# Performance work log

Hardware: AMD Instinct MI355X
Metric: run time of the kernel (lower is better)

The kernel has to match this reference:

```python
import jax, jax.numpy as jnp
import numpy as np

B, T, N, C, H, S = 8, 24, 2048, 64, 8, 4
HD = C // H
EPS_NORM = 1e-12   # torch F.normalize eps
EPS_DEN = 1e-5     # clamp_min in fast_attention
LN_EPS = 1e-5
SCALE1 = 0.01      # self.scale[1]


def _ln(x, g, b):
    m = x.mean(-1, keepdims=True)
    v = ((x - m) ** 2).mean(-1, keepdims=True)
    return (x - m) * jax.lax.rsqrt(v + LN_EPS) * g + b


def _fast_attn(q, k, v):
    # q,k,v: [b, l, h, m] ; performer-style linear attention with L2-normalized feature maps
    q = q / jnp.maximum(jnp.linalg.norm(q, axis=-1, keepdims=True), EPS_NORM)
    k = k / jnp.maximum(jnp.linalg.norm(k, axis=-1, keepdims=True), EPS_NORM)
    L = q.shape[1]
    kvs = jnp.einsum('blhm,blhd->bhmd', k, v)
    num = jnp.einsum('bnhm,bhmd->bnhd', q, kvs) + L * v
    den = jnp.einsum('bnhm,bhm->bnh', q, k.sum(axis=1))[..., None] + L
    return num / jnp.maximum(den, EPS_DEN)  # [b, l, h, d]


def _attn_layer(x, qkv_w, out_w, out_b):
    # x: [B, T, N, C]; spatial (over N) + temporal (over T) linear attention, concat, project
    b, t, n, c = x.shape
    qkv = x @ qkv_w.T                      # [b,t,n,3c], no bias (qkv_bias=False)
    q, k, v = jnp.split(qkv, 3, axis=-1)
    sh = lambda a: a.reshape(b * t, n, H, HD)                    # flatten (B,T) -> attend over nodes
    th = lambda a: a.swapaxes(1, 2).reshape(b * n, t, H, HD)     # flatten (B,N) -> attend over time
    out_s = _fast_attn(sh(q), sh(k), sh(v)).reshape(b, t, n, c)
    out_t = _fast_attn(th(q), th(k), th(v)).reshape(b, n, t, c).swapaxes(1, 2)
    return jnp.concatenate([out_s, out_t], axis=-1) @ out_w.T + out_b


def setup_inputs() -> dict:
    key = jax.random.key(0)
    ks = jax.random.split(key, 20)
    stdv = 1.0 / np.sqrt(N)
    w = 0.02
    inp = {
        'x': jax.random.normal(ks[0], (B, T, N, C), jnp.float32),
        'phi': jax.random.normal(ks[1], (S, N, N), jnp.float32) * (N ** -0.5),
        'phi_inv': jax.random.normal(ks[2], (S, N, N), jnp.float32) * (N ** -0.5),
        'diag_w': jax.random.uniform(ks[3], (S, N), jnp.float32, -stdv, stdv),
        'qkv0_w': jax.random.normal(ks[4], (3 * C, C), jnp.float32) * w,
        'out0_w': jax.random.normal(ks[5], (C, 2 * C), jnp.float32) * w,
        'out0_b': jnp.zeros((C,), jnp.float32),
        'qkv1_w': jax.random.normal(ks[6], (3 * C, C), jnp.float32) * w,
        'out1_w': jax.random.normal(ks[7], (C, 2 * C), jnp.float32) * w,
        'out1_b': jnp.zeros((C,), jnp.float32),
        'pw0_w': jax.random.normal(ks[8], (C, C), jnp.float32) * w,
        'pw0_b': jax.random.normal(ks[9], (C,), jnp.float32) * w,
        'pw1_w': jax.random.normal(ks[10], (C, C), jnp.float32) * w,
        'pw1_b': jax.random.normal(ks[11], (C,), jnp.float32) * w,
        'fc1_w': jax.random.normal(ks[12], (2 * C, C), jnp.float32) * w,
        'fc1_b': jnp.zeros((2 * C,), jnp.float32),
        'fc2_w': jax.random.normal(ks[13], (C, 2 * C), jnp.float32) * w,
        'fc2_b': jnp.zeros((C,), jnp.float32),
        'ln1_g': jnp.ones((C,), jnp.float32),
        'ln1_b': jnp.zeros((C,), jnp.float32),
        'ln2_g': jnp.ones((C,), jnp.float32),
        'ln2_b': jnp.zeros((C,), jnp.float32),
    }
    return inp


def reference(x, phi, phi_inv, diag_w, qkv0_w, out0_w, out0_b, qkv1_w, out1_w, out1_b,
              pw0_w, pw0_b, pw1_w, pw1_b, fc1_w, fc1_b, fc2_w, fc2_b,
              ln1_g, ln1_b, ln2_g, ln2_b):
    # Graph wavelet propagate (order=2): x_list = [x, W(x)] with
    # W(x)[b,t,n,c] = sum_j (sum_s phi_s diag(diag_w_s) phi_inv_s)[n,j] x[b,t,j,c]
    Msum = jnp.einsum('sij,sj,sjk->ik', phi, diag_w, phi_inv)   # [N,N]
    x_k = jnp.einsum('nj,btjc->btnc', Msum, x)
    att0 = _attn_layer(x, qkv0_w, out0_w, out0_b)
    att1 = _attn_layer(x_k, qkv1_w, out1_w, out1_b)
    # scale = [1, 0.01]; c starts as x, then becomes att0
    x_glo = x + att0 * (x @ pw0_w.T + pw0_b) + att1 * (att0 @ pw1_w.T + pw1_b) * SCALE1
    # In torch, x_glo aliases x (in-place +=), so ln1(x + x_glo) == ln1(2 * x_glo)
    y = _ln(2.0 * x_glo, ln1_g, ln1_b)
    h = jax.nn.relu(y @ fc1_w.T + fc1_b) @ fc2_w.T + fc2_b
    return _ln(y + h, ln2_g, ln2_b)
```

## Files before the change

kernel.cpp:

```cpp
#include <hip/hip_runtime.h>

typedef unsigned short u16;
typedef unsigned int u32;
typedef __attribute__((ext_vector_type(8))) __bf16 bf16x8;
typedef __attribute__((ext_vector_type(4))) float floatx4;

#define TB 24
#define NN 2048
#define QC 192

__device__ __forceinline__ float b2f(u16 v) { return __uint_as_float(((u32)v) << 16); }
__device__ __forceinline__ u16 f2bu(float f) {
  u32 u = __float_as_uint(f);
  u32 r = (u + 0x7fffu + ((u >> 16) & 1u)) >> 16;
  return (u16)r;
}
__device__ __forceinline__ u32 packpair(float a, float b) {
  return (u32)f2bu(a) | ((u32)f2bu(b) << 16);
}
__device__ __forceinline__ void unpack8(uint4 v, float* f) {
  f[0] = __uint_as_float(v.x << 16); f[1] = __uint_as_float(v.x & 0xffff0000u);
  f[2] = __uint_as_float(v.y << 16); f[3] = __uint_as_float(v.y & 0xffff0000u);
  f[4] = __uint_as_float(v.z << 16); f[5] = __uint_as_float(v.z & 0xffff0000u);
  f[6] = __uint_as_float(v.w << 16); f[7] = __uint_as_float(v.w & 0xffff0000u);
}
__device__ __forceinline__ float wredsum(float v) {
#pragma unroll
  for (int m = 32; m > 0; m >>= 1) v += __shfl_xor(v, m, 64);
  return v;
}

__global__ __launch_bounds__(256) void cast_weights(
    const float* __restrict__ q0, const float* __restrict__ q1,
    const float* __restrict__ o0, const float* __restrict__ o1,
    const float* __restrict__ p0, const float* __restrict__ p1,
    const float* __restrict__ f1, const float* __restrict__ f2,
    u16* __restrict__ dst) {
  int i = blockIdx.x * 256 + threadIdx.x;
  float v;
  if (i < 12288) v = q0[i];
  else if (i < 24576) v = q1[i - 12288];
  else if (i < 32768) v = o0[i - 24576];
  else if (i < 40960) v = o1[i - 32768];
  else if (i < 45056) v = p0[i - 40960];
  else if (i < 49152) v = p1[i - 45056];
  else if (i < 57344) v = f1[i - 49152];
  else v = f2[i - 57344];
  dst[i] = f2bu(v);
}

__global__ __launch_bounds__(256) void cast_bulk(const float* __restrict__ src,
                                                 u16* __restrict__ dst) {
  long i = ((long)blockIdx.x * 256 + threadIdx.x) * 8;
  float4 a = *(const float4*)(src + i);
  float4 b = *(const float4*)(src + i + 4);
  uint4 o = uint4{packpair(a.x, a.y), packpair(a.z, a.w),
                  packpair(b.x, b.y), packpair(b.z, b.w)};
  *(uint4*)(dst + i) = o;
}

__global__ __launch_bounds__(256) void prep_pt(const float* __restrict__ phi_inv,
                                               const float* __restrict__ diag,
                                               u16* __restrict__ PT) {
  const int s = blockIdx.z;
  const float* phi_inv_s = phi_inv + (long)s * 4194304;
  const float* diag_s = diag + (long)s * 2048;
  u16* PTs = PT + (long)s * 4194304;
  const long i0 = (long)blockIdx.x * 64, j0 = (long)blockIdx.y * 64;
  __shared__ float tile[64][65];
  for (int t = threadIdx.x; t < 512; t += 256) {
    int r = t >> 3, c8 = (t & 7) << 3;
    float dv = diag_s[j0 + r];
    const float* sp = phi_inv_s + (j0 + r) * 2048 + i0 + c8;
    float4 p = *(const float4*)sp;
    float4 q = *(const float4*)(sp + 4);
    tile[r][c8 + 0] = p.x * dv; tile[r][c8 + 1] = p.y * dv;
    tile[r][c8 + 2] = p.z * dv; tile[r][c8 + 3] = p.w * dv;
    tile[r][c8 + 4] = q.x * dv; tile[r][c8 + 5] = q.y * dv;
    tile[r][c8 + 6] = q.z * dv; tile[r][c8 + 7] = q.w * dv;
  }
  __syncthreads();
  for (int t = threadIdx.x; t < 512; t += 256) {
    int r = t >> 3, c8 = (t & 7) << 3;
    uint4 o;
    o.x = packpair(tile[c8 + 0][r], tile[c8 + 1][r]);
    o.y = packpair(tile[c8 + 2][r], tile[c8 + 3][r]);
    o.z = packpair(tile[c8 + 4][r], tile[c8 + 5][r]);
    o.w = packpair(tile[c8 + 6][r], tile[c8 + 7][r]);
    *(uint4*)(PTs + (i0 + r) * 2048 + j0 + c8) = o;
  }
}

__global__ __launch_bounds__(256) void prep_xt(const float* __restrict__ x,
                                               u16* __restrict__ XT) {
  const int bt = blockIdx.y;
  const long j0 = (long)blockIdx.x * 64;
  __shared__ float tile[64][65];
  const float* src = x + (long)bt * NN * 64;
  for (int t = threadIdx.x; t < 512; t += 256) {
    int r = t >> 3, c8 = (t & 7) << 3;
    const float* sp = src + (j0 + r) * 64 + c8;
    float4 p = *(const float4*)sp;
    float4 q = *(const float4*)(sp + 4);
    tile[r][c8 + 0] = p.x; tile[r][c8 + 1] = p.y;
    tile[r][c8 + 2] = p.z; tile[r][c8 + 3] = p.w;
    tile[r][c8 + 4] = q.x; tile[r][c8 + 5] = q.y;
    tile[r][c8 + 6] = q.z; tile[r][c8 + 7] = q.w;
  }
  __syncthreads();
  u16* dst = XT + (long)bt * 64 * NN;
  for (int t = threadIdx.x; t < 512; t += 256) {
    int r = t >> 3, c8 = (t & 7) << 3;
    uint4 o;
    o.x = packpair(tile[c8 + 0][r], tile[c8 + 1][r]);
    o.y = packpair(tile[c8 + 2][r], tile[c8 + 3][r]);
    o.z = packpair(tile[c8 + 4][r], tile[c8 + 5][r]);
    o.w = packpair(tile[c8 + 6][r], tile[c8 + 7][r]);
    *(uint4*)(dst + (long)r * 2048 + j0 + c8) = o;
  }
}

template <int MODE>
__global__ __launch_bounds__(256) void gemm128(
    const u16* __restrict__ A, const u16* __restrict__ Bt, void* __restrict__ C,
    int K, int lda, int ldb, int ldc, int nseg, long aseg, long bseg) {
  __shared__ __align__(16) u16 As[128 * 64];
  __shared__ __align__(16) u16 Bs[128 * 64];
  const int tid = threadIdx.x;
  const int wave = tid >> 6, lane = tid & 63;
  const int l15 = lane & 15, lq = lane >> 4;
  const int wr = wave >> 1, wc = wave & 1;
  const long m0 = (long)blockIdx.x * 128;
  const long n0 = (long)blockIdx.y * 128;
  const int rl = lane >> 3;
  const int csw = (lane & 7) ^ rl;
  floatx4 acc[4][4];
#pragma unroll
  for (int a = 0; a < 4; a++)
#pragma unroll
    for (int b = 0; b < 4; b++) acc[a][b] = floatx4{0.f, 0.f, 0.f, 0.f};
  for (int s = 0; s < nseg; s++) {
    const u16* Ab = A + s * aseg;
    const u16* Bb = Bt + s * bseg;
    for (int k0 = 0; k0 < K; k0 += 64) {
      __syncthreads();
#pragma unroll
      for (int la = 0; la < 4; la++) {
        const int ldx = wave * 4 + la;
        const int rowt = ldx * 8 + rl;
        const u16* ga = Ab + (m0 + rowt) * (long)lda + k0 + csw * 8;
        const u16* gb = Bb + (n0 + rowt) * (long)ldb + k0 + csw * 8;
        __builtin_amdgcn_global_load_lds(
            (const __attribute__((address_space(1))) void*)ga,
            (__attribute__((address_space(3))) void*)(As + ldx * 512), 16, 0, 0);
        __builtin_amdgcn_global_load_lds(
            (const __attribute__((address_space(1))) void*)gb,
            (__attribute__((address_space(3))) void*)(Bs + ldx * 512), 16, 0, 0);
      }
      __syncthreads();
#pragma unroll
      for (int ks = 0; ks < 2; ks++) {
        bf16x8 af[4], bf[4];
        const int cp = ((ks * 4 + lq) ^ (l15 & 7)) * 8;
#pragma unroll
        for (int t = 0; t < 4; t++) {
          af[t] = *(const bf16x8*)(As + (wr * 64 + t * 16 + l15) * 64 + cp);
          bf[t] = *(const bf16x8*)(Bs + (wc * 64 + t * 16 + l15) * 64 + cp);
        }
#pragma unroll
        for (int ti = 0; ti < 4; ti++)
#pragma unroll
          for (int tj = 0; tj < 4; tj++)
            acc[ti][tj] = __builtin_amdgcn_mfma_f32_16x16x32_bf16(
                af[ti], bf[tj], acc[ti][tj], 0, 0, 0);
      }
    }
  }
#pragma unroll
  for (int ti = 0; ti < 4; ti++) {
#pragma unroll
    for (int tj = 0; tj < 4; tj++) {
#pragma unroll
      for (int i = 0; i < 4; i++) {
        const long row = m0 + wr * 64 + ti * 16 + lq * 4 + i;
        const long col = n0 + wc * 64 + tj * 16 + l15;
        if (MODE == 0) {
          ((u16*)C)[row * ldc + col] = f2bu(acc[ti][tj][i]);
        } else {
          ((float*)C)[(col >> 6) * 131072L + row * 64 + (col & 63)] = acc[ti][tj][i];
        }
      }
    }
  }
}

template <bool AF32, bool CF32>
__global__ __launch_bounds__(256) void gemm_bt(
    const void* __restrict__ A, const u16* __restrict__ Bt, void* __restrict__ C,
    int K, int lda, int ldb, int ldc, int nseg, long aseg, long bseg,
    long bbstride, long cbstride, int accum) {
  __shared__ __align__(16) u16 Asm[64][72];
  __shared__ __align__(16) u16 Bsm[64][72];
  const int tid = threadIdx.x;
  const int wave = tid >> 6, lane = tid & 63;
  const int l15 = lane & 15, lq = lane >> 4;
  const long m0 = (long)blockIdx.x * 64;
  const long n0 = (long)blockIdx.y * 64;
  const long bz = blockIdx.z;
  const int srow = tid >> 3;
  const int scol = (tid & 7) << 3;
  floatx4 acc[4];
#pragma unroll
  for (int t = 0; t < 4; t++) acc[t] = floatx4{0.f, 0.f, 0.f, 0.f};
  for (int s = 0; s < nseg; s++) {
    const u16* Bb = Bt + s * bseg + bz * bbstride;
    for (int k0 = 0; k0 < K; k0 += 64) {
      __syncthreads();
      uint4 a0, a1;
      if (AF32) {
        const float* Af = (const float*)A + s * aseg;
        const float* p0 = Af + (m0 + srow) * lda + k0 + scol;
        const float* p1 = Af + (m0 + srow + 32) * lda + k0 + scol;
        float4 x0 = *(const float4*)p0, x1 = *(const float4*)(p0 + 4);
        float4 y0 = *(const float4*)p1, y1 = *(const float4*)(p1 + 4);
        a0 = uint4{packpair(x0.x, x0.y), packpair(x0.z, x0.w),
                   packpair(x1.x, x1.y), packpair(x1.z, x1.w)};
        a1 = uint4{packpair(y0.x, y0.y), packpair(y0.z, y0.w),
                   packpair(y1.x, y1.y), packpair(y1.z, y1.w)};
      } else {
        const u16* Ab = (const u16*)A + s * aseg;
        a0 = *(const uint4*)(Ab + (m0 + srow) * lda + k0 + scol);
        a1 = *(const uint4*)(Ab + (m0 + srow + 32) * lda + k0 + scol);
      }
      uint4 b0 = *(const uint4*)(Bb + (n0 + srow) * ldb + k0 + scol);
      uint4 b1 = *(const uint4*)(Bb + (n0 + srow + 32) * ldb + k0 + scol);
      *(uint4*)(&Asm[srow][scol]) = a0;
      *(uint4*)(&Asm[srow + 32][scol]) = a1;
      *(uint4*)(&Bsm[srow][scol]) = b0;
      *(uint4*)(&Bsm[srow + 32][scol]) = b1;
      __syncthreads();
#pragma unroll
      for (int ks = 0; ks < 2; ks++) {
        bf16x8 af = *(const bf16x8*)(&Asm[wave * 16 + l15][ks * 32 + lq * 8]);
#pragma unroll
        for (int t = 0; t < 4; t++) {
          bf16x8 bfr = *(const bf16x8*)(&Bsm[t * 16 + l15][ks * 32 + lq * 8]);
          acc[t] = __builtin_amdgcn_mfma_f32_16x16x32_bf16(af, bfr, acc[t], 0, 0, 0);
        }
      }
    }
  }
#pragma unroll
  for (int t = 0; t < 4; t++) {
#pragma unroll
    for (int i = 0; i < 4; i++) {
      long off = (m0 + wave * 16 + lq * 4 + i) * ldc + n0 + t * 16 + l15;
      float v = acc[t][i];
      if (CF32) {
        float* Cb = (float*)C + bz * cbstride;
        if (accum) v += Cb[off];
        Cb[off] = v;
      } else {
        u16* Cb = (u16*)C + bz * cbstride;
        if (accum) v += b2f(Cb[off]);
        Cb[off] = f2bu(v);
      }
    }
  }
}

template <int K, int LDA, int NOUT, int LDO, bool BIAS, bool RELU, bool AF32, bool OF32>
__global__ __launch_bounds__(256) void skinny_gemm(const void* __restrict__ In,
                                                   const u16* __restrict__ W,
                                                   const float* __restrict__ Bv,
                                                   void* __restrict__ Out) {
  constexpr int NT = NOUT / 16;
  const int lane = threadIdx.x & 63;
  const int wave = threadIdx.x >> 6;
  const int l15 = lane & 15, lq = lane >> 4;
  const long m0 = ((long)blockIdx.x * 4 + wave) * 16;
  floatx4 acc[NT];
#pragma unroll
  for (int t = 0; t < NT; t++) acc[t] = floatx4{0.f, 0.f, 0.f, 0.f};
#pragma unroll
  for (int k0 = 0; k0 < K; k0 += 32) {
    bf16x8 af;
    if (AF32) {
      const float* arow = (const float*)In + (m0 + l15) * (long)LDA + lq * 8;
      float4 p = *(const float4*)(arow + k0);
      float4 q = *(const float4*)(arow + k0 + 4);
      uint4 pk = uint4{packpair(p.x, p.y), packpair(p.z, p.w),
                       packpair(q.x, q.y), packpair(q.z, q.w)};
      af = __builtin_bit_cast(bf16x8, pk);
    } else {
      const u16* arow = (const u16*)In + (m0 + l15) * (long)LDA + lq * 8;
      af = *(const bf16x8*)(arow + k0);
    }
#pragma unroll
    for (int t = 0; t < NT; t++) {
      bf16x8 bfr = *(const bf16x8*)(W + (t * 16 + l15) * K + k0 + lq * 8);
      acc[t] = __builtin_amdgcn_mfma_f32_16x16x32_bf16(af, bfr, acc[t], 0, 0, 0);
    }
  }
#pragma unroll
  for (int t = 0; t < NT; t++) {
    float bv = BIAS ? Bv[t * 16 + l15] : 0.f;
#pragma unroll
    for (int i = 0; i < 4; i++) {
      float v = acc[t][i] + bv;
      if (RELU) v = fmaxf(v, 0.f);
      long off = (m0 + lq * 4 + i) * (long)LDO + t * 16 + l15;
      if (OF32) ((float*)Out)[off] = v;
      else ((u16*)Out)[off] = f2bu(v);
    }
  }
}

__global__ __launch_bounds__(256) void spat_stats(const u16* __restrict__ Q,
                                                  float* __restrict__ stats) {
  const int bh = blockIdx.x;
  const int bt = bh >> 3, h = bh & 7;
  const int tid = threadIdx.x, lane = tid & 63, wave = tid >> 6;
  float kvs[8][8], ksm[8];
#pragma unroll
  for (int m = 0; m < 8; m++) {
    ksm[m] = 0.f;
#pragma unroll
    for (int d = 0; d < 8; d++) kvs[m][d] = 0.f;
  }
  const u16* base = Q + (long)bt * NN * QC + 64 + h * 8;
  for (int l = tid; l < NN; l += 256) {
    const u16* p = base + (long)l * QC;
    float kv[8], vv[8];
    unpack8(*(const uint4*)p, kv);
    unpack8(*(const uint4*)(p + 64), vv);
    float nr = 0.f;
#pragma unroll
    for (int m = 0; m < 8; m++) nr += kv[m] * kv[m];
    float inv = 1.f / fmaxf(sqrtf(nr), 1e-12f);
#pragma unroll
    for (int m = 0; m < 8; m++) {
      float km = kv[m] * inv;
      ksm[m] += km;
#pragma unroll
      for (int d = 0; d < 8; d++) kvs[m][d] += km * vv[d];
    }
  }
  __shared__ float red[4][72];
#pragma unroll
  for (int m = 0; m < 8; m++) {
    ksm[m] = wredsum(ksm[m]);
#pragma unroll
    for (int d = 0; d < 8; d++) kvs[m][d] = wredsum(kvs[m][d]);
  }
  if (lane == 0) {
#pragma unroll
    for (int m = 0; m < 8; m++) {
      red[wave][64 + m] = ksm[m];
#pragma unroll
      for (int d = 0; d < 8; d++) red[wave][m * 8 + d] = kvs[m][d];
    }
  }
  __syncthreads();
  if (tid < 72) {
    stats[(long)bh * 72 + tid] = red[0][tid] + red[1][tid] + red[2][tid] + red[3][tid];
  }
}

__global__ __launch_bounds__(256) void temp_attn(u16* __restrict__ Q) {
  const long g = (long)blockIdx.x * 256 + threadIdx.x;
  const int h = (int)(g & 7);
  const long bn = g >> 3;
  const int n = (int)(bn & 2047);
  const int b = (int)(bn >> 11);
  u16* qb = Q + ((long)b * TB * NN + n) * QC + h * 8;
  const long ts = (long)NN * QC;
  float kvs[8][8], ksm[8];
#pragma unroll
  for (int m = 0; m < 8; m++) {
    ksm[m] = 0.f;
#pragma unroll
    for (int d = 0; d < 8; d++) kvs[m][d] = 0.f;
  }
  for (int t = 0; t < TB; t++) {
    const u16* p = qb + t * ts;
    float kv[8], vv[8];
    unpack8(*(const uint4*)(p + 64), kv);
    unpack8(*(const uint4*)(p + 128), vv);
    float nr = 0.f;
#pragma unroll
    for (int m = 0; m < 8; m++) nr += kv[m] * kv[m];
    float inv = 1.f / fmaxf(sqrtf(nr), 1e-12f);
#pragma unroll
    for (int m = 0; m < 8; m++) {
      float km = kv[m] * inv;
      ksm[m] += km;
#pragma unroll
      for (int d = 0; d < 8; d++) kvs[m][d] += km * vv[d];
    }
  }
  for (int t = 0; t < TB; t++) {
    u16* p = qb + t * ts;
    float qv[8], vv[8];
    unpack8(*(const uint4*)p, qv);
    unpack8(*(const uint4*)(p + 128), vv);
    float nr = 0.f;
#pragma unroll
    for (int m = 0; m < 8; m++) nr += qv[m] * qv[m];
    float inv = 1.f / fmaxf(sqrtf(nr), 1e-12f);
    float num[8];
    float den = 24.f;
#pragma unroll
    for (int d = 0; d < 8; d++) num[d] = 24.f * vv[d];
#pragma unroll
    for (int m = 0; m < 8; m++) {
      float qm = qv[m] * inv;
      den += qm * ksm[m];
#pragma unroll
      for (int d = 0; d < 8; d++) num[d] += qm * kvs[m][d];
    }
    den = fmaxf(den, 1e-5f);
    float id = 1.f / den;
    uint4 o;
    o.x = packpair(num[0] * id, num[1] * id);
    o.y = packpair(num[2] * id, num[3] * id);
    o.z = packpair(num[4] * id, num[5] * id);
    o.w = packpair(num[6] * id, num[7] * id);
    *(uint4*)(p + 64) = o;
  }
}

__global__ __launch_bounds__(256) void spat_out(u16* __restrict__ Q,
                                                const float* __restrict__ stats) {
  const long g = (long)blockIdx.x * 256 + threadIdx.x;
  const int h = (int)(g & 7);
  const long r = g >> 3;
  const int bt = (int)(r >> 11);
  u16* p = Q + r * QC + h * 8;
  float qv[8], vv[8];
  unpack8(*(const uint4*)p, qv);
  unpack8(*(const uint4*)(p + 128), vv);
  const float* st = stats + ((long)bt * 8 + h) * 72;
  float nr = 0.f;
#pragma unroll
  for (int m = 0; m < 8; m++) nr += qv[m] * qv[m];
  float inv = 1.f / fmaxf(sqrtf(nr), 1e-12f);
  const float L = 2048.f;
  float num[8];
#pragma unroll
  for (int d = 0; d < 8; d++) num[d] = L * vv[d];
  float den = L;
#pragma unroll
  for (int m = 0; m < 8; m++) {
    float qm = qv[m] * inv;
    den += qm * st[64 + m];
#pragma unroll
    for (int d = 0; d < 8; d++) num[d] += qm * st[m * 8 + d];
  }
  den = fmaxf(den, 1e-5f);
  float id = 1.f / den;
  uint4 o;
  o.x = packpair(num[0] * id, num[1] * id);
  o.y = packpair(num[2] * id, num[3] * id);
  o.z = packpair(num[4] * id, num[5] * id);
  o.w = packpair(num[6] * id, num[7] * id);
  *(uint4*)p = o;
}

__global__ __launch_bounds__(256) void combine_ln(
    const float* __restrict__ x, const u16* __restrict__ a0p, int sa0,
    const float* __restrict__ a1p, const u16* __restrict__ P0, int sp0,
    const u16* __restrict__ P1, int sp1, const float* __restrict__ g1,
    const float* __restrict__ b1, u16* __restrict__ Y) {
  const long r = (long)blockIdx.x * 4 + (threadIdx.x >> 6);
  const int d = threadIdx.x & 63;
  float xv = x[r * 64 + d];
  float a0 = b2f(a0p[r * sa0 + d]);
  float a1 = a1p[r * 64 + d];
  float p0 = b2f(P0[r * sp0 + d]);
  float p1 = b2f(P1[r * sp1 + d]);
  float t = 2.f * (xv + a0 * p0 + a1 * p1 * 0.01f);
  float mu = wredsum(t) * 0.015625f;
  float dv = t - mu;
  float var = wredsum(dv * dv) * 0.015625f;
  float y = dv * rsqrtf(var + 1e-5f) * g1[d] + b1[d];
  Y[r * 64 + d] = f2bu(y);
}

__global__ __launch_bounds__(256) void final_ln(const u16* __restrict__ Yp,
                                                const u16* __restrict__ Op,
                                                const float* __restrict__ g2,
                                                const float* __restrict__ b2p,
                                                float* __restrict__ out) {
  const long r = (long)blockIdx.x * 4 + (threadIdx.x >> 6);
  const int d = threadIdx.x & 63;
  const long o = r * 64 + d;
  float t = b2f(Yp[o]) + b2f(Op[o]);
  float mu = wredsum(t) * 0.015625f;
  float dv = t - mu;
  float var = wredsum(dv * dv) * 0.015625f;
  out[o] = dv * rsqrtf(var + 1e-5f) * g2[d] + b2p[d];
}

extern "C" void kernel_launch(void* const* d_in, const int* in_sizes, int n_in,
                              void* d_out, int out_size, void* d_ws, size_t ws_size,
                              hipStream_t stream) {
  const float* x = (const float*)d_in[0];
  const float* phi = (const float*)d_in[1];
  const float* phiinv = (const float*)d_in[2];
  const float* diagw = (const float*)d_in[3];
  const float* qkv0w = (const float*)d_in[4];
  const float* out0w = (const float*)d_in[5];
  const float* out0b = (const float*)d_in[6];
  const float* qkv1w = (const float*)d_in[7];
  const float* out1w = (const float*)d_in[8];
  const float* out1b = (const float*)d_in[9];
  const float* pw0w = (const float*)d_in[10];
  const float* pw0b = (const float*)d_in[11];
  const float* pw1w = (const float*)d_in[12];
  const float* pw1b = (const float*)d_in[13];
  const float* fc1w = (const float*)d_in[14];
  const float* fc1b = (const float*)d_in[15];
  const float* fc2w = (const float*)d_in[16];
  const float* fc2b = (const float*)d_in[17];
  const float* ln1g = (const float*)d_in[18];
  const float* ln1b = (const float*)d_in[19];
  const float* ln2g = (const float*)d_in[20];
  const float* ln2b = (const float*)d_in[21];

  const long per = 25221120L;
  int CH = 1;
  if ((long)ws_size >= 262144L + 8 * per) CH = 8;
  else if ((long)ws_size >= 262144L + 4 * per) CH = 4;
  else if ((long)ws_size >= 262144L + 2 * per) CH = 2;
  const int NCH = 8 / CH;

  char* ws = (char*)d_ws;
  u16* wb = (u16*)ws;
  u16* wq0 = wb + 0;
  u16* wq1 = wb + 12288;
  u16* wo0 = wb + 24576;
  u16* wo1 = wb + 32768;
  u16* wp0 = wb + 40960;
  u16* wp1 = wb + 45056;
  u16* wf1 = wb + 49152;
  u16* wf2 = wb + 57344;
  const long B0 = 262144L;
  u16* Ms = (u16*)(ws + B0);
  u16* PT = (u16*)(ws + B0 + 8388608L);
  u16* PB = (u16*)(ws + B0 + 41943040L);
  u16* XT = (u16*)(ws + B0 + 8388608L);
  u16* Q = (u16*)(ws + B0);
  float* st = (float*)(ws + B0 + (long)CH * 18874368L);
  u16* Yb = (u16*)(ws + B0 + (long)CH * 18929664L);
  u16* Hb = (u16*)(ws + B0);
  u16* Ob = (u16*)(ws + B0 + (long)CH * 12582912L);
  float* dof = (float*)d_out;

  cast_weights<<<256, 256, 0, stream>>>(qkv0w, qkv1w, out0w, out1w, pw0w, pw1w,
                                        fc1w, fc2w, wb);

  if (CH == 8) {
    prep_pt<<<dim3(32, 32, 4), 256, 0, stream>>>(phiinv, diagw, PT);
    cast_bulk<<<8192, 256, 0, stream>>>(phi, PB);
    gemm128<0><<<dim3(16, 16), 256, 0, stream>>>(PB, PT, Ms, 2048, 2048, 2048,
                                                 2048, 4, 4194304L, 4194304L);
    prep_xt<<<dim3(32, 192), 256, 0, stream>>>(x, XT);
    gemm128<1><<<dim3(16, 96), 256, 0, stream>>>(Ms, XT, dof, 2048, 2048, 2048, 0,
                                                 1, 0L, 0L);
  } else {
    for (int s = 0; s < 4; s++) {
      prep_pt<<<dim3(32, 32, 1), 256, 0, stream>>>(phiinv + (long)s * 4194304,
                                                   diagw + (long)s * 2048, PT);
      gemm_bt<true, false><<<dim3(32, 32, 1), 256, 0, stream>>>(
          phi + (long)s * 4194304, PT, Ms, 2048, 2048, 2048, 2048, 1, 0L, 0L, 0L,
          0L, s ? 1 : 0);
    }
    for (int c = 0; c < NCH; c++) {
      long eoff = (long)c * CH * 49152 * 64;
      prep_xt<<<dim3(32, CH * 24), 256, 0, stream>>>(x + eoff, XT);
      gemm_bt<false, true><<<dim3(32, 1, CH * 24), 256, 0, stream>>>(
          Ms, XT, dof + eoff, 2048, 2048, 2048, 64, 1, 0L, 0L, 131072L, 131072L, 0);
    }
  }
  for (int c = 0; c < NCH; c++) {
    long eoff = (long)c * CH * 49152 * 64;
    skinny_gemm<64, 64, 192, 192, false, false, true, false>
        <<<CH * 768, 256, 0, stream>>>(dof + eoff, wq1, nullptr, Q);
    spat_stats<<<CH * 192, 256, 0, stream>>>(Q, st);
    temp_attn<<<CH * 64, 256, 0, stream>>>(Q);
    spat_out<<<CH * 1536, 256, 0, stream>>>(Q, st);
    skinny_gemm<128, 192, 64, 64, true, false, false, true>
        <<<CH * 768, 256, 0, stream>>>(Q, wo1, out1b, dof + eoff);
  }
  for (int c = 0; c < NCH; c++) {
    long eoff = (long)c * CH * 49152 * 64;
    const float* x_c = x + eoff;
    skinny_gemm<64, 64, 192, 192, false, false, true, false>
        <<<CH * 768, 256, 0, stream>>>(x_c, wq0, nullptr, Q);
    spat_stats<<<CH * 192, 256, 0, stream>>>(Q, st);
    temp_attn<<<CH * 64, 256, 0, stream>>>(Q);
    spat_out<<<CH * 1536, 256, 0, stream>>>(Q, st);
    skinny_gemm<128, 192, 64, 192, true, false, false, false>
        <<<CH * 768, 256, 0, stream>>>(Q, wo0, out0b, Q + 128);
    skinny_gemm<64, 64, 64, 192, true, false, true, false>
        <<<CH * 768, 256, 0, stream>>>(x_c, wp0, pw0b, Q);
    skinny_gemm<64, 192, 64, 192, true, false, false, false>
        <<<CH * 768, 256, 0, stream>>>(Q + 128, wp1, pw1b, Q + 64);
    combine_ln<<<CH * 12288, 256, 0, stream>>>(x_c, Q + 128, 192, dof + eoff, Q, 192,
                                               Q + 64, 192, ln1g, ln1b, Yb);
    skinny_gemm<64, 64, 128, 128, true, true, false, false>
        <<<CH * 768, 256, 0, stream>>>(Yb, wf1, fc1b, Hb);
    skinny_gemm<128, 128, 64, 64, true, false, false, false>
        <<<CH * 768, 256, 0, stream>>>(Hb, wf2, fc2b, Ob);
    final_ln<<<CH * 12288, 256, 0, stream>>>(Yb, Ob, ln2g, ln2b, dof + eoff);
  }
}
```

Before: 1.624 ms.

## Fuse attention and LN stages, split Msum GEMM over segments, store activations as bf16

```diff
diff --git a/kernel.cpp b/kernel.cpp
--- a/kernel.cpp
+++ b/kernel.cpp
@@ -27,6 +27,11 @@
 __device__ __forceinline__ float wredsum(float v) {
 #pragma unroll
   for (int m = 32; m > 0; m >>= 1) v += __shfl_xor(v, m, 64);
+  return v;
+}
+__device__ __forceinline__ float red16(float v) {
+#pragma unroll
+  for (int m = 8; m > 0; m >>= 1) v += __shfl_xor(v, m, 64);
   return v;
 }
 
@@ -92,7 +97,8 @@
 }
 
 __global__ __launch_bounds__(256) void prep_xt(const float* __restrict__ x,
-                                               u16* __restrict__ XT) {
+                                               u16* __restrict__ XT,
+                                               u16* __restrict__ XB) {
   const int bt = blockIdx.y;
   const long j0 = (long)blockIdx.x * 64;
   __shared__ float tile[64][65];
@@ -106,6 +112,11 @@
     tile[r][c8 + 2] = p.z; tile[r][c8 + 3] = p.w;
     tile[r][c8 + 4] = q.x; tile[r][c8 + 5] = q.y;
     tile[r][c8 + 6] = q.z; tile[r][c8 + 7] = q.w;
+    if (XB) {
+      uint4 o = uint4{packpair(p.x, p.y), packpair(p.z, p.w),
+                      packpair(q.x, q.y), packpair(q.z, q.w)};
+      *(uint4*)(XB + (long)bt * 131072 + (j0 + r) * 64 + c8) = o;
+    }
   }
   __syncthreads();
   u16* dst = XT + (long)bt * 64 * NN;
@@ -130,8 +141,13 @@
   const int wave = tid >> 6, lane = tid & 63;
   const int l15 = lane & 15, lq = lane >> 4;
   const int wr = wave >> 1, wc = wave & 1;
-  const long m0 = (long)blockIdx.x * 128;
-  const long n0 = (long)blockIdx.y * 128;
+  const int nbx = gridDim.x;
+  const int nwg = nbx * gridDim.y;
+  int id = blockIdx.x + nbx * blockIdx.y;
+  id = (id & 7) * (nwg >> 3) + (id >> 3);
+  const long m0 = (long)(id % nbx) * 128;
+  const long n0 = (long)(id / nbx) * 128;
+  const long zo = (MODE == 2) ? (long)blockIdx.z : 0;
   const int rl = lane >> 3;
   const int csw = (lane & 7) ^ rl;
   floatx4 acc[4][4];
@@ -140,8 +156,8 @@
 #pragma unroll
     for (int b = 0; b < 4; b++) acc[a][b] = floatx4{0.f, 0.f, 0.f, 0.f};
   for (int s = 0; s < nseg; s++) {
-    const u16* Ab = A + s * aseg;
-    const u16* Bb = Bt + s * bseg;
+    const u16* Ab = A + (s + zo) * aseg;
+    const u16* Bb = Bt + (s + zo) * bseg;
     for (int k0 = 0; k0 < K; k0 += 64) {
       __syncthreads();
 #pragma unroll
@@ -186,12 +202,40 @@
         const long col = n0 + wc * 64 + tj * 16 + l15;
         if (MODE == 0) {
           ((u16*)C)[row * ldc + col] = f2bu(acc[ti][tj][i]);
+        } else if (MODE == 1) {
+          ((float*)C)[(col >> 6) * 131072L + row * 64 + (col & 63)] = acc[ti][tj][i];
+        } else if (MODE == 2) {
+          ((float*)C)[zo * 4194304L + row * (long)ldc + col] = acc[ti][tj][i];
         } else {
-          ((float*)C)[(col >> 6) * 131072L + row * 64 + (col & 63)] = acc[ti][tj][i];
+          ((u16*)C)[(col >> 6) * 131072L + row * 64 + (col & 63)] =
+              f2bu(acc[ti][tj][i]);
         }
       }
     }
   }
+}
+
+__global__ __launch_bounds__(256) void reduce_ms(const float* __restrict__ P,
+                                                 u16* __restrict__ M) {
+  long i = ((long)blockIdx.x * 256 + threadIdx.x) * 8;
+  float s[8];
+  {
+    float4 a = *(const float4*)(P + i);
+    float4 b = *(const float4*)(P + i + 4);
+    s[0] = a.x; s[1] = a.y; s[2] = a.z; s[3] = a.w;
+    s[4] = b.x; s[5] = b.y; s[6] = b.z; s[7] = b.w;
+  }
+#pragma unroll
+  for (int z = 1; z < 4; z++) {
+    const float* p = P + (long)z * 4194304L + i;
+    float4 a = *(const float4*)p;
+    float4 b = *(const float4*)(p + 4);
+    s[0] += a.x; s[1] += a.y; s[2] += a.z; s[3] += a.w;
+    s[4] += b.x; s[5] += b.y; s[6] += b.z; s[7] += b.w;
+  }
+  uint4 o = uint4{packpair(s[0], s[1]), packpair(s[2], s[3]),
+                  packpair(s[4], s[5]), packpair(s[6], s[7])};
+  *(uint4*)(M + i) = o;
 }
 
 template <bool AF32, bool CF32>
@@ -318,7 +362,9 @@
 
 __global__ __launch_bounds__(256) void spat_stats(const u16* __restrict__ Q,
                                                   float* __restrict__ stats) {
-  const int bh = blockIdx.x;
+  const int nb = gridDim.x;
+  int blk = blockIdx.x;
+  const int bh = ((nb & 7) == 0) ? ((blk & 7) * (nb >> 3) + (blk >> 3)) : blk;
   const int bt = bh >> 3, h = bh & 7;
   const int tid = threadIdx.x, lane = tid & 63, wave = tid >> 6;
   float kvs[8][8], ksm[8];
@@ -427,6 +473,84 @@
     o.z = packpair(num[4] * id, num[5] * id);
     o.w = packpair(num[6] * id, num[7] * id);
     *(uint4*)(p + 64) = o;
+  }
+}
+
+__global__ __launch_bounds__(256) void temp_spat(u16* __restrict__ Q,
+                                                 const float* __restrict__ stats) {
+  const long g = (long)blockIdx.x * 256 + threadIdx.x;
+  const int h = (int)(g & 7);
+  const long bn = g >> 3;
+  const int n = (int)(bn & 2047);
+  const int b = (int)(bn >> 11);
+  u16* qb = Q + ((long)b * TB * NN + n) * QC + h * 8;
+  const long ts = (long)NN * QC;
+  float kvs[8][8], ksm[8];
+#pragma unroll
+  for (int m = 0; m < 8; m++) {
+    ksm[m] = 0.f;
+#pragma unroll
+    for (int d = 0; d < 8; d++) kvs[m][d] = 0.f;
+  }
+  for (int t = 0; t < TB; t++) {
+    const u16* p = qb + t * ts;
+    float kv[8], vv[8];
+    unpack8(*(const uint4*)(p + 64), kv);
+    unpack8(*(const uint4*)(p + 128), vv);
+    float nr = 0.f;
+#pragma unroll
+    for (int m = 0; m < 8; m++) nr += kv[m] * kv[m];
+    float inv = 1.f / fmaxf(sqrtf(nr), 1e-12f);
+#pragma unroll
+    for (int m = 0; m < 8; m++) {
+      float km = kv[m] * inv;
+      ksm[m] += km;
+#pragma unroll
+      for (int d = 0; d < 8; d++) kvs[m][d] += km * vv[d];
+    }
+  }
+  const float* stb = stats + ((long)b * TB * 8 + h) * 72;
+  for (int t = 0; t < TB; t++) {
+    u16* p = qb + t * ts;
+    const float* st = stb + (long)t * 576;
+    float qv[8], vv[8];
+    unpack8(*(const uint4*)p, qv);
+    unpack8(*(const uint4*)(p + 128), vv);
+    float nr = 0.f;
+#pragma unroll
+    for (int m = 0; m < 8; m++) nr += qv[m] * qv[m];
+    float inv = 1.f / fmaxf(sqrtf(nr), 1e-12f);
+    float numt[8], nums[8];
+    float dent = 24.f, dens = 2048.f;
+#pragma unroll
+    for (int d = 0; d < 8; d++) {
+      numt[d] = 24.f * vv[d];
+      nums[d] = 2048.f * vv[d];
+    }
+#pragma unroll
+    for (int m = 0; m < 8; m++) {
+      float qm = qv[m] * inv;
+      dent += qm * ksm[m];
+      dens += qm * st[64 + m];
+#pragma unroll
+      for (int d = 0; d < 8; d++) {
+        numt[d] += qm * kvs[m][d];
+        nums[d] += qm * st[m * 8 + d];
+      }
+    }
+    float idt = 1.f / fmaxf(dent, 1e-5f);
+    float ids = 1.f / fmaxf(dens, 1e-5f);
+    uint4 os, ot;
+    os.x = packpair(nums[0] * ids, nums[1] * ids);
+    os.y = packpair(nums[2] * ids, nums[3] * ids);
+    os.z = packpair(nums[4] * ids, nums[5] * ids);
+    os.w = packpair(nums[6] * ids, nums[7] * ids);
+    ot.x = packpair(numt[0] * idt, numt[1] * idt);
+    ot.y = packpair(numt[2] * idt, numt[3] * idt);
+    ot.z = packpair(numt[4] * idt, numt[5] * idt);
+    ot.w = packpair(numt[6] * idt, numt[7] * idt);
+    *(uint4*)p = os;
+    *(uint4*)(p + 64) = ot;
   }
 }
 
@@ -465,6 +589,120 @@
   o.z = packpair(num[4] * id, num[5] * id);
   o.w = packpair(num[6] * id, num[7] * id);
   *(uint4*)p = o;
+}
+
+__global__ __launch_bounds__(256) void pw1_combine_ln(
+    const u16* __restrict__ Q, const u16* __restrict__ W,
+    const float* __restrict__ Bv, const float* __restrict__ x,
+    const u16* __restrict__ a1, const float* __restrict__ g1,
+    const float* __restrict__ b1, u16* __restrict__ Y) {
+  const int lane = threadIdx.x & 63;
+  const int wave = threadIdx.x >> 6;
+  const int l15 = lane & 15, lq = lane >> 4;
+  const long m0 = ((long)blockIdx.x * 4 + wave) * 16;
+  floatx4 acc[4];
+#pragma unroll
+  for (int t = 0; t < 4; t++) acc[t] = floatx4{0.f, 0.f, 0.f, 0.f};
+#pragma unroll
+  for (int k0 = 0; k0 < 64; k0 += 32) {
+    bf16x8 af = *(const bf16x8*)(Q + (m0 + l15) * 192 + 128 + k0 + lq * 8);
+#pragma unroll
+    for (int t = 0; t < 4; t++) {
+      bf16x8 bfr = *(const bf16x8*)(W + (t * 16 + l15) * 64 + k0 + lq * 8);
+      acc[t] = __builtin_amdgcn_mfma_f32_16x16x32_bf16(af, bfr, acc[t], 0, 0, 0);
+    }
+  }
+  float tv[4][4];
+#pragma unroll
+  for (int t = 0; t < 4; t++) {
+    const int col = t * 16 + l15;
+    const float bv = Bv[col];
+#pragma unroll
+    for (int i = 0; i < 4; i++) {
+      const long row = m0 + lq * 4 + i;
+      float p1v = acc[t][i] + bv;
+      float xv = x[row * 64 + col];
+      float a0 = b2f(Q[row * 192 + 128 + col]);
+      float p0 = b2f(Q[row * 192 + col]);
+      float a1v = b2f(a1[row * 64 + col]);
+      tv[t][i] = 2.f * (xv + a0 * p0 + a1v * p1v * 0.01f);
+    }
+  }
+#pragma unroll
+  for (int i = 0; i < 4; i++) {
+    float s = tv[0][i] + tv[1][i] + tv[2][i] + tv[3][i];
+    s = red16(s);
+    float mu = s * 0.015625f;
+    float vs = 0.f;
+#pragma unroll
+    for (int t = 0; t < 4; t++) {
+      float d = tv[t][i] - mu;
+      vs += d * d;
+    }
+    vs = red16(vs);
+    float rs = rsqrtf(vs * 0.015625f + 1e-5f);
+    const long row = m0 + lq * 4 + i;
+#pragma unroll
+    for (int t = 0; t < 4; t++) {
+      const int col = t * 16 + l15;
+      float y = (tv[t][i] - mu) * rs * g1[col] + b1[col];
+      Y[row * 64 + col] = f2bu(y);
+    }
+  }
+}
+
+__global__ __launch_bounds__(256) void fc2_ln(
+    const u16* __restrict__ Hb, const u16* __restrict__ W,
+    const float* __restrict__ Bv, const u16* __restrict__ Yb,
+    const float* __restrict__ g2, const float* __restrict__ b2v,
+    float* __restrict__ out) {
+  const int lane = threadIdx.x & 63;
+  const int wave = threadIdx.x >> 6;
+  const int l15 = lane & 15, lq = lane >> 4;
+  const long m0 = ((long)blockIdx.x * 4 + wave) * 16;
+  floatx4 acc[4];
+#pragma unroll
+  for (int t = 0; t < 4; t++) acc[t] = floatx4{0.f, 0.f, 0.f, 0.f};
+#pragma unroll
+  for (int k0 = 0; k0 < 128; k0 += 32) {
+    bf16x8 af = *(const bf16x8*)(Hb + (m0 + l15) * 128 + k0 + lq * 8);
+#pragma unroll
+    for (int t = 0; t < 4; t++) {
+      bf16x8 bfr = *(const bf16x8*)(W + (t * 16 + l15) * 128 + k0 + lq * 8);
+      acc[t] = __builtin_amdgcn_mfma_f32_16x16x32_bf16(af, bfr, acc[t], 0, 0, 0);
+    }
+  }
+  float tv[4][4];
+#pragma unroll
+  for (int t = 0; t < 4; t++) {
+    const int col = t * 16 + l15;
+    const float bv = Bv[col];
+#pragma unroll
+    for (int i = 0; i < 4; i++) {
+      const long row = m0 + lq * 4 + i;
+      tv[t][i] = acc[t][i] + bv + b2f(Yb[row * 64 + col]);
+    }
+  }
+#pragma unroll
+  for (int i = 0; i < 4; i++) {
+    float s = tv[0][i] + tv[1][i] + tv[2][i] + tv[3][i];
+    s = red16(s);
+    float mu = s * 0.015625f;
+    float vs = 0.f;
+#pragma unroll
+    for (int t = 0; t < 4; t++) {
+      float d = tv[t][i] - mu;
+      vs += d * d;
+    }
+    vs = red16(vs);
+    float rs = rsqrtf(vs * 0.015625f + 1e-5f);
+    const long row = m0 + lq * 4 + i;
+#pragma unroll
+    for (int t = 0; t < 4; t++) {
+      const int col = t * 16 + l15;
+      out[row * 64 + col] = (tv[t][i] - mu) * rs * g2[col] + b2v[col];
+    }
+  }
 }
 
 __global__ __launch_bounds__(256) void combine_ln(
@@ -546,29 +784,61 @@
   u16* wf1 = wb + 49152;
   u16* wf2 = wb + 57344;
   const long B0 = 262144L;
-  u16* Ms = (u16*)(ws + B0);
-  u16* PT = (u16*)(ws + B0 + 8388608L);
-  u16* PB = (u16*)(ws + B0 + 41943040L);
-  u16* XT = (u16*)(ws + B0 + 8388608L);
-  u16* Q = (u16*)(ws + B0);
-  float* st = (float*)(ws + B0 + (long)CH * 18874368L);
-  u16* Yb = (u16*)(ws + B0 + (long)CH * 18929664L);
-  u16* Hb = (u16*)(ws + B0);
-  u16* Ob = (u16*)(ws + B0 + (long)CH * 12582912L);
   float* dof = (float*)d_out;
 
   cast_weights<<<256, 256, 0, stream>>>(qkv0w, qkv1w, out0w, out1w, pw0w, pw1w,
                                         fc1w, fc2w, wb);
 
   if (CH == 8) {
+    u16* PT = (u16*)(ws + B0);
+    u16* PB = (u16*)(ws + B0 + 33554432L);
+    float* MsP = (float*)(ws + B0 + 67108864L);
+    u16* Ms = (u16*)(ws + B0 + 134217728L);
+    u16* XT = (u16*)(ws + B0);
+    u16* XB = (u16*)(ws + B0 + 151437312L);
+    u16* Q = (u16*)(ws + B0);
+    float* st = (float*)(ws + B0 + 150994944L);
+    u16* Yb = XB;
+    u16* Hb = (u16*)(ws + B0);
+    u16* xkb = (u16*)d_out;
+    u16* a1b = xkb + 25165824L;
+
     prep_pt<<<dim3(32, 32, 4), 256, 0, stream>>>(phiinv, diagw, PT);
     cast_bulk<<<8192, 256, 0, stream>>>(phi, PB);
-    gemm128<0><<<dim3(16, 16), 256, 0, stream>>>(PB, PT, Ms, 2048, 2048, 2048,
-                                                 2048, 4, 4194304L, 4194304L);
-    prep_xt<<<dim3(32, 192), 256, 0, stream>>>(x, XT);
-    gemm128<1><<<dim3(16, 96), 256, 0, stream>>>(Ms, XT, dof, 2048, 2048, 2048, 0,
+    gemm128<2><<<dim3(16, 16, 4), 256, 0, stream>>>(PB, PT, MsP, 2048, 2048, 2048,
+                                                    2048, 1, 4194304L, 4194304L);
+    reduce_ms<<<2048, 256, 0, stream>>>(MsP, Ms);
+    prep_xt<<<dim3(32, 192), 256, 0, stream>>>(x, XT, XB);
+    gemm128<3><<<dim3(16, 96), 256, 0, stream>>>(Ms, XT, xkb, 2048, 2048, 2048, 0,
                                                  1, 0L, 0L);
+    skinny_gemm<64, 64, 192, 192, false, false, false, false>
+        <<<6144, 256, 0, stream>>>(xkb, wq1, nullptr, Q);
+    spat_stats<<<1536, 256, 0, stream>>>(Q, st);
+    temp_spat<<<512, 256, 0, stream>>>(Q, st);
+    skinny_gemm<128, 192, 64, 64, true, false, false, false>
+        <<<6144, 256, 0, stream>>>(Q, wo1, out1b, a1b);
+    skinny_gemm<64, 64, 192, 192, false, false, false, false>
+        <<<6144, 256, 0, stream>>>(XB, wq0, nullptr, Q);
+    spat_stats<<<1536, 256, 0, stream>>>(Q, st);
+    temp_spat<<<512, 256, 0, stream>>>(Q, st);
+    skinny_gemm<128, 192, 64, 192, true, false, false, false>
+        <<<6144, 256, 0, stream>>>(Q, wo0, out0b, Q + 128);
+    skinny_gemm<64, 64, 64, 192, true, false, false, false>
+        <<<6144, 256, 0, stream>>>(XB, wp0, pw0b, Q);
+    pw1_combine_ln<<<6144, 256, 0, stream>>>(Q, wp1, pw1b, x, a1b, ln1g, ln1b, Yb);
+    skinny_gemm<64, 64, 128, 128, true, true, false, false>
+        <<<6144, 256, 0, stream>>>(Yb, wf1, fc1b, Hb);
+    fc2_ln<<<6144, 256, 0, stream>>>(Hb, wf2, fc2b, Yb, ln2g, ln2b, dof);
   } else {
+    u16* Ms = (u16*)(ws + B0);
+    u16* PT = (u16*)(ws + B0 + 8388608L);
+    u16* XT = (u16*)(ws + B0 + 8388608L);
+    u16* Q = (u16*)(ws + B0);
+    float* st = (float*)(ws + B0 + (long)CH * 18874368L);
+    u16* Yb = (u16*)(ws + B0 + (long)CH * 18929664L);
+    u16* Hb = (u16*)(ws + B0);
+    u16* Ob = (u16*)(ws + B0 + (long)CH * 12582912L);
+
     for (int s = 0; s < 4; s++) {
       prep_pt<<<dim3(32, 32, 1), 256, 0, stream>>>(phiinv + (long)s * 4194304,
                                                    diagw + (long)s * 2048, PT);
@@ -578,41 +848,41 @@
     }
     for (int c = 0; c < NCH; c++) {
       long eoff = (long)c * CH * 49152 * 64;
-      prep_xt<<<dim3(32, CH * 24), 256, 0, stream>>>(x + eoff, XT);
+      prep_xt<<<dim3(32, CH * 24), 256, 0, stream>>>(x + eoff, XT, nullptr);
       gemm_bt<false, true><<<dim3(32, 1, CH * 24), 256, 0, stream>>>(
           Ms, XT, dof + eoff, 2048, 2048, 2048, 64, 1, 0L, 0L, 131072L, 131072L, 0);
     }
-  }
-  for (int c = 0; c < NCH; c++) {
-    long eoff = (long)c * CH * 49152 * 64;
-    skinny_gemm<64, 64, 192, 192, false, false, true, false>
-        <<<CH * 768, 256, 0, stream>>>(dof + eoff, wq1, nullptr, Q);
-    spat_stats<<<CH * 192, 256, 0, stream>>>(Q, st);
-    temp_attn<<<CH * 64, 256, 0, stream>>>(Q);
-    spat_out<<<CH * 1536, 256, 0, stream>>>(Q, st);
-    skinny_gemm<128, 192, 64, 64, true, false, false, true>
-        <<<CH * 768, 256, 0, stream>>>(Q, wo1, out1b, dof + eoff);
-  }
-  for (int c = 0; c < NCH; c++) {
-    long eoff = (long)c * CH * 49152 * 64;
-    const float* x_c = x + eoff;
-    skinny_gemm<64, 64, 192, 192, false, false, true, false>
-        <<<CH * 768, 256, 0, stream>>>(x_c, wq0, nullptr, Q);
-    spat_stats<<<CH * 192, 256, 0, stream>>>(Q, st);
-    temp_attn<<<CH * 64, 256, 0, stream>>>(Q);
-    spat_out<<<CH * 1536, 256, 0, stream>>>(Q, st);
-    skinny_gemm<128, 192, 64, 192, true, false, false, false>
-        <<<CH * 768, 256, 0, stream>>>(Q, wo0, out0b, Q + 128);
-    skinny_gemm<64, 64, 64, 192, true, false, true, false>
-        <<<CH * 768, 256, 0, stream>>>(x_c, wp0, pw0b, Q);
-    skinny_gemm<64, 192, 64, 192, true, false, false, false>
-        <<<CH * 768, 256, 0, stream>>>(Q + 128, wp1, pw1b, Q + 64);
-    combine_ln<<<CH * 12288, 256, 0, stream>>>(x_c, Q + 128, 192, dof + eoff, Q, 192,
-                                               Q + 64, 192, ln1g, ln1b, Yb);
-    skinny_gemm<64, 64, 128, 128, true, true, false, false>
-        <<<CH * 768, 256, 0, stream>>>(Yb, wf1, fc1b, Hb);
-    skinny_gemm<128, 128, 64, 64, true, false, false, false>
-        <<<CH * 768, 256, 0, stream>>>(Hb, wf2, fc2b, Ob);
-    final_ln<<<CH * 12288, 256, 0, stream>>>(Yb, Ob, ln2g, ln2b, dof + eoff);
-  }
-}
+    for (int c = 0; c < NCH; c++) {
+      long eoff = (long)c * CH * 49152 * 64;
+      skinny_gemm<64, 64, 192, 192, false, false, true, false>
+          <<<CH * 768, 256, 0, stream>>>(dof + eoff, wq1, nullptr, Q);
+      spat_stats<<<CH * 192, 256, 0, stream>>>(Q, st);
+      temp_attn<<<CH * 64, 256, 0, stream>>>(Q);
+      spat_out<<<CH * 1536, 256, 0, stream>>>(Q, st);
+      skinny_gemm<128, 192, 64, 64, true, false, false, true>
+          <<<CH * 768, 256, 0, stream>>>(Q, wo1, out1b, dof + eoff);
+    }
+    for (int c = 0; c < NCH; c++) {
+      long eoff = (long)c * CH * 49152 * 64;
+      const float* x_c = x + eoff;
+      skinny_gemm<64, 64, 192, 192, false, false, true, false>
+          <<<CH * 768, 256, 0, stream>>>(x_c, wq0, nullptr, Q);
+      spat_stats<<<CH * 192, 256, 0, stream>>>(Q, st);
+      temp_attn<<<CH * 64, 256, 0, stream>>>(Q);
+      spat_out<<<CH * 1536, 256, 0, stream>>>(Q, st);
+      skinny_gemm<128, 192, 64, 192, true, false, false, false>
+          <<<CH * 768, 256, 0, stream>>>(Q, wo0, out0b, Q + 128);
+      skinny_gemm<64, 64, 64, 192, true, false, true, false>
+          <<<CH * 768, 256, 0, stream>>>(x_c, wp0, pw0b, Q);
+      skinny_gemm<64, 192, 64, 192, true, false, false, false>
+          <<<CH * 768, 256, 0, stream>>>(Q + 128, wp1, pw1b, Q + 64);
+      combine_ln<<<CH * 12288, 256, 0, stream>>>(x_c, Q + 128, 192, dof + eoff, Q,
+                                                 192, Q + 64, 192, ln1g, ln1b, Yb);
+      skinny_gemm<64, 64, 128, 128, true, true, false, false>
+          <<<CH * 768, 256, 0, stream>>>(Yb, wf1, fc1b, Hb);
+      skinny_gemm<128, 128, 64, 64, true, false, false, false>
+          <<<CH * 768, 256, 0, stream>>>(Hb, wf2, fc2b, Ob);
+      final_ln<<<CH * 12288, 256, 0, stream>>>(Yb, Ob, ln2g, ln2b, dof + eoff);
+    }
+  }
+}
```

Measured after the change: 1.339 ms. 1.21x faster.
